# Kernel tuning notes

Hardware: AMD Instinct MI355X
Metric: run time of the kernel (lower is better)

## Reference

```python
import jax, jax.numpy as jnp
import numpy as np
import math

B, S, HID, H = 4, 1024, 1024, 16
DH = HID // H

def setup_inputs() -> dict:
    key = jax.random.key(0)
    ks = jax.random.split(key, 16)
    inp = {
        'q': jax.random.normal(ks[0], (B, S, HID), jnp.float32),
        'k': jax.random.normal(ks[1], (B, S, HID), jnp.float32),
        'v': jax.random.normal(ks[2], (B, S, HID), jnp.float32),
        'k_b': jax.random.normal(ks[3], (B, S, HID), jnp.float32),
        'mask': jax.random.randint(ks[4], (B, S), 0, 2, jnp.int32),
    }
    sc = 1.0 / math.sqrt(HID)
    names = ['Wq', 'Wk', 'Wv', 'Wkb', 'Wo']
    for i, n in enumerate(names):
        inp[n] = jax.random.normal(ks[5 + i], (HID, HID), jnp.float32) * sc
        inp['b' + n[1:]] = jnp.zeros((HID,), jnp.float32)
    return inp

def _split_heads(x):
    # [B,S,HID] -> [B,H,S,DH]
    return x.reshape(B, S, H, DH).transpose(0, 2, 1, 3)

def reference(q, k, v, k_b, mask, Wq, bq, Wk, bk, Wv, bv, Wkb, bkb, Wo, bo):
    qh = _split_heads(q @ Wq.T + bq)
    kh = _split_heads(k @ Wk.T + bk)
    vh = _split_heads(v @ Wv.T + bv)
    kbh = _split_heads(k_b @ Wkb.T + bkb)
    scale = 1.0 / math.sqrt(3 * DH)
    # Q@K^T + Q@Kb^T == Q@(K+Kb)^T
    corr = jnp.einsum('bhsd,bhtd->bhst', qh, kh + kbh) * scale
    # mask[b,j] broadcast over heads and query positions
    corr = jnp.where(mask[:, None, None, :] == 0, jnp.float32(-1e9), corr)
    prob = jax.nn.softmax(corr, axis=-1)  # dropout p=0 (eval)
    hidden = jnp.einsum('bhst,bhtd->bhsd', prob, vh)
    hidden = hidden.transpose(0, 2, 1, 3).reshape(B, S, HID)
    return hidden @ Wo.T + bo
```

## Files before the change

kernel.cpp:

```cpp
#include <hip/hip_runtime.h>
#include <hip/hip_bf16.h>
#include <stdint.h>

#define B_   4
#define S_   1024
#define HID_ 1024
#define H_   16
#define DH_  64

typedef short bf16x8 __attribute__((ext_vector_type(8)));
typedef float f32x4  __attribute__((ext_vector_type(4)));
typedef unsigned int u32;
typedef unsigned short u16;

typedef u32 __attribute__((address_space(1))) as1_u32;
typedef u32 __attribute__((address_space(3))) as3_u32;

__device__ __forceinline__ f32x4 mfma16(bf16x8 a, bf16x8 b, f32x4 c) {
  return __builtin_amdgcn_mfma_f32_16x16x32_bf16(a, b, c, 0, 0, 0);
}

__device__ __forceinline__ void gload16(const void* g, void* l) {
  __builtin_amdgcn_global_load_lds((const as1_u32*)g, (as3_u32*)l, 16, 0, 0);
}

__device__ __forceinline__ u16 f2bf(float f) {
  __hip_bfloat16 h = __float2bfloat16(f);
  union { __hip_bfloat16 h; u16 u; } cv; cv.h = h; return cv.u;
}

__device__ __forceinline__ u32 cvtpk(float lo, float hi) {
  u32 r;
  asm("v_cvt_pk_bf16_f32 %0, %1, %2" : "=v"(r) : "v"(lo), "v"(hi));
  return r;
}

__global__ __launch_bounds__(256) void cvt_all(
    const float* a0, const float* a1, const float* a2, const float* a3,
    const float* w0, const float* w1, const float* w2, const float* w3, const float* w4,
    u16* da0, u16* da1, u16* da2, u16* da3,
    u16* dw0, u16* dw1, u16* dw2, u16* dw3, u16* dw4) {
  int bb = blockIdx.x;
  const float* s; u16* d; size_t i;
  if (bb < 8192) {
    int t = bb * 256 + threadIdx.x;
    int sel = t >> 19;
    i = (size_t)(t & 524287) * 8;
    if (sel == 0)      { s = a0; d = da0; }
    else if (sel == 1) { s = a1; d = da1; }
    else if (sel == 2) { s = a2; d = da2; }
    else               { s = a3; d = da3; }
  } else {
    int t = (bb - 8192) * 256 + threadIdx.x;
    int sel = t >> 17;
    i = (size_t)(t & 131071) * 8;
    if (sel == 0)      { s = w0; d = dw0; }
    else if (sel == 1) { s = w1; d = dw1; }
    else if (sel == 2) { s = w2; d = dw2; }
    else if (sel == 3) { s = w3; d = dw3; }
    else               { s = w4; d = dw4; }
  }
  float4 v0 = *(const float4*)(s + i);
  float4 v1 = *(const float4*)(s + i + 4);
  uint4 r;
  r.x = cvtpk(v0.x, v0.y);
  r.y = cvtpk(v0.z, v0.w);
  r.z = cvtpk(v1.x, v1.y);
  r.w = cvtpk(v1.z, v1.w);
  *(uint4*)(d + i) = r;
}

__global__ __launch_bounds__(256) void gemm_proj(
    const u16* __restrict__ qbf, const u16* __restrict__ Wqbf,
    const u16* __restrict__ kbf, const u16* __restrict__ Wkbf,
    const u16* __restrict__ kbbf, const u16* __restrict__ Wkbbf,
    const u16* __restrict__ vbf, const u16* __restrict__ Wvbf,
    const float* __restrict__ bq, const float* __restrict__ bk,
    const float* __restrict__ bkb, const float* __restrict__ bv,
    u16* __restrict__ Qp, u16* __restrict__ KKp, u16* __restrict__ Vtp) {
  __shared__ __align__(16) char smem[32768];
  const int tid = threadIdx.x;
  const int lane = tid & 63, w = tid >> 6;
  const int g = lane >> 4, ql = lane & 15;
  const int wm = w >> 1, wn = w & 1;
  const int xr = ql & 7;
  const int logical = (blockIdx.x & 7) * 128 + (blockIdx.x >> 3);

  if (logical < 512) {
    const int m0 = (logical >> 4) * 128;
    const int n0 = (logical & 15) * 64;
    f32x4 acc[4][2];
    #pragma unroll
    for (int mi = 0; mi < 4; ++mi)
      #pragma unroll
      for (int ni = 0; ni < 2; ++ni) acc[mi][ni] = f32x4{0.f, 0.f, 0.f, 0.f};

    for (int kt = 0; kt < 32; ++kt) {
      const u16* As = (kt < 16) ? kbf : kbbf;
      const u16* Ws = (kt < 16) ? Wkbf : Wkbbf;
      const int kk = (kt & 15) * 64;
      #pragma unroll
      for (int is = 0; is < 4; ++is) {
        int o = is * 4096 + tid * 16;
        int row = o >> 7, ch = (o >> 4) & 7;
        gload16(As + (size_t)(m0 + row) * HID_ + kk + ((ch ^ (row & 7)) * 8),
                smem + is * 4096 + w * 1024);
      }
      #pragma unroll
      for (int is = 0; is < 2; ++is) {
        int o = is * 4096 + tid * 16;
        int row = o >> 7, ch = (o >> 4) & 7;
        gload16(Ws + (size_t)(n0 + row) * HID_ + kk + ((ch ^ (row & 7)) * 8),
                smem + 16384 + is * 4096 + w * 1024);
      }
      __syncthreads();
      bf16x8 af[4][2], bfv[2][2];
      #pragma unroll
      for (int mi = 0; mi < 4; ++mi)
        #pragma unroll
        for (int c = 0; c < 2; ++c) {
          int row = wm * 64 + mi * 16 + ql;
          af[mi][c] = *(const bf16x8*)(smem + row * 128 + (((c * 4 + g) ^ xr) * 16));
        }
      #pragma unroll
      for (int ni = 0; ni < 2; ++ni)
        #pragma unroll
        for (int c = 0; c < 2; ++c) {
          int row = wn * 32 + ni * 16 + ql;
          bfv[ni][c] = *(const bf16x8*)(smem + 16384 + row * 128 + (((c * 4 + g) ^ xr) * 16));
        }
      #pragma unroll
      for (int c = 0; c < 2; ++c)
        #pragma unroll
        for (int mi = 0; mi < 4; ++mi)
          #pragma unroll
          for (int ni = 0; ni < 2; ++ni)
            acc[mi][ni] = mfma16(af[mi][c], bfv[ni][c], acc[mi][ni]);
      __syncthreads();
    }
    #pragma unroll
    for (int ni = 0; ni < 2; ++ni) {
      int n = n0 + wn * 32 + ni * 16 + ql;
      float bs = bk[n] + bkb[n];
      #pragma unroll
      for (int mi = 0; mi < 4; ++mi)
        #pragma unroll
        for (int i = 0; i < 4; ++i) {
          int m = m0 + wm * 64 + mi * 16 + g * 4 + i;
          KKp[(size_t)m * HID_ + n] = f2bf(acc[mi][ni][i] + bs);
        }
    }
    return;
  }

  const int unit = (logical - 512) >> 8;
  const int bidu = logical & 255;
  const int m0 = (bidu >> 3) * 128;
  const int n0 = (bidu & 7) * 128;
  const u16* A0 = unit ? vbf : qbf;
  const u16* W0 = unit ? Wvbf : Wqbf;
  const float* b0 = unit ? bv : bq;
  const float osc = unit ? 1.f : 0.07216878364870322f * 1.44269504088896340f;

  f32x4 acc[4][4];
  #pragma unroll
  for (int mi = 0; mi < 4; ++mi)
    #pragma unroll
    for (int ni = 0; ni < 4; ++ni) acc[mi][ni] = f32x4{0.f, 0.f, 0.f, 0.f};

  for (int kt = 0; kt < 16; ++kt) {
    const int kk = kt * 64;
    #pragma unroll
    for (int is = 0; is < 4; ++is) {
      int o = is * 4096 + tid * 16;
      int row = o >> 7, ch = (o >> 4) & 7;
      gload16(A0 + (size_t)(m0 + row) * HID_ + kk + ((ch ^ (row & 7)) * 8),
              smem + is * 4096 + w * 1024);
      gload16(W0 + (size_t)(n0 + row) * HID_ + kk + ((ch ^ (row & 7)) * 8),
              smem + 16384 + is * 4096 + w * 1024);
    }
    __syncthreads();
    bf16x8 af[4][2], bfv[4][2];
    #pragma unroll
    for (int mi = 0; mi < 4; ++mi)
      #pragma unroll
      for (int c = 0; c < 2; ++c) {
        int row = wm * 64 + mi * 16 + ql;
        af[mi][c] = *(const bf16x8*)(smem + row * 128 + (((c * 4 + g) ^ xr) * 16));
      }
    #pragma unroll
    for (int ni = 0; ni < 4; ++ni)
      #pragma unroll
      for (int c = 0; c < 2; ++c) {
        int row = wn * 64 + ni * 16 + ql;
        bfv[ni][c] = *(const bf16x8*)(smem + 16384 + row * 128 + (((c * 4 + g) ^ xr) * 16));
      }
    #pragma unroll
    for (int c = 0; c < 2; ++c)
      #pragma unroll
      for (int mi = 0; mi < 4; ++mi)
        #pragma unroll
        for (int ni = 0; ni < 4; ++ni)
          acc[mi][ni] = mfma16(af[mi][c], bfv[ni][c], acc[mi][ni]);
    __syncthreads();
  }

  if (unit == 0) {
    #pragma unroll
    for (int ni = 0; ni < 4; ++ni) {
      int n = n0 + wn * 64 + ni * 16 + ql;
      float bs = b0[n];
      #pragma unroll
      for (int mi = 0; mi < 4; ++mi)
        #pragma unroll
        for (int i = 0; i < 4; ++i) {
          int m = m0 + wm * 64 + mi * 16 + g * 4 + i;
          Qp[(size_t)m * HID_ + n] = f2bf((acc[mi][ni][i] + bs) * osc);
        }
    }
  } else {
    char* tp = smem + w * 8192;
    #pragma unroll
    for (int ni = 0; ni < 4; ++ni) {
      int n = n0 + wn * 64 + ni * 16 + ql;
      float bs = b0[n];
      #pragma unroll
      for (int mi = 0; mi < 4; ++mi)
        #pragma unroll
        for (int i = 0; i < 4; ++i) {
          int nl = ni * 16 + ql;
          int ml = mi * 16 + g * 4 + i;
          *(u16*)(tp + nl * 128 + (((ml >> 3) ^ (nl & 7)) * 16) + (ml & 7) * 2) =
              f2bf(acc[mi][ni][i] + bs);
        }
    }
    __syncthreads();
    int nl = lane;
    int n = n0 + wn * 64 + nl;
    int h = n >> 6, dh = n & 63;
    int mb = m0 + wm * 64;
    int b = mb >> 10, s0 = mb & 1023;
    int bh = b * H_ + h;
    u16* orow = Vtp + (((size_t)(bh * DH_ + dh)) << 10) + s0;
    #pragma unroll
    for (int j = 0; j < 8; ++j) {
      uint4 val = *(const uint4*)(tp + nl * 128 + ((j ^ (nl & 7)) * 16));
      *(uint4*)(orow + j * 8) = val;
    }
  }
}

__global__ __launch_bounds__(256) void gemm_o(const u16* __restrict__ A0, const u16* __restrict__ W0,
                                              const float* __restrict__ bias0, float* __restrict__ outp) {
  __shared__ __align__(16) char smem[24576];
  const int tid = threadIdx.x;
  const int lane = tid & 63, w = tid >> 6;
  const int g = lane >> 4, ql = lane & 15;
  const int wm = w >> 1, wn = w & 1;
  const int logical = (blockIdx.x & 7) * 64 + (blockIdx.x >> 3);
  const int m0 = (logical >> 4) * 128;
  const int n0 = (logical & 15) * 64;
  const int xr = ql & 7;

  f32x4 acc[4][2];
  #pragma unroll
  for (int mi = 0; mi < 4; ++mi)
    #pragma unroll
    for (int ni = 0; ni < 2; ++ni) acc[mi][ni] = f32x4{0.f, 0.f, 0.f, 0.f};

  for (int kt = 0; kt < 16; ++kt) {
    const int kk = kt * 64;
    #pragma unroll
    for (int is = 0; is < 4; ++is) {
      int o = is * 4096 + tid * 16;
      int row = o >> 7, ch = (o >> 4) & 7;
      gload16(A0 + (size_t)(m0 + row) * HID_ + kk + ((ch ^ (row & 7)) * 8),
              smem + is * 4096 + w * 1024);
    }
    #pragma unroll
    for (int is = 0; is < 2; ++is) {
      int o = is * 4096 + tid * 16;
      int row = o >> 7, ch = (o >> 4) & 7;
      gload16(W0 + (size_t)(n0 + row) * HID_ + kk + ((ch ^ (row & 7)) * 8),
              smem + 16384 + is * 4096 + w * 1024);
    }
    __syncthreads();
    bf16x8 af[4][2], bfv[2][2];
    #pragma unroll
    for (int mi = 0; mi < 4; ++mi)
      #pragma unroll
      for (int c = 0; c < 2; ++c) {
        int row = wm * 64 + mi * 16 + ql;
        af[mi][c] = *(const bf16x8*)(smem + row * 128 + (((c * 4 + g) ^ xr) * 16));
      }
    #pragma unroll
    for (int ni = 0; ni < 2; ++ni)
      #pragma unroll
      for (int c = 0; c < 2; ++c) {
        int row = wn * 32 + ni * 16 + ql;
        bfv[ni][c] = *(const bf16x8*)(smem + 16384 + row * 128 + (((c * 4 + g) ^ xr) * 16));
      }
    #pragma unroll
    for (int c = 0; c < 2; ++c)
      #pragma unroll
      for (int mi = 0; mi < 4; ++mi)
        #pragma unroll
        for (int ni = 0; ni < 2; ++ni)
          acc[mi][ni] = mfma16(af[mi][c], bfv[ni][c], acc[mi][ni]);
    __syncthreads();
  }

  #pragma unroll
  for (int ni = 0; ni < 2; ++ni) {
    int n = n0 + wn * 32 + ni * 16 + ql;
    float bs = bias0[n];
    #pragma unroll
    for (int mi = 0; mi < 4; ++mi)
      #pragma unroll
      for (int i = 0; i < 4; ++i) {
        int m = m0 + wm * 64 + mi * 16 + g * 4 + i;
        outp[(size_t)m * HID_ + n] = acc[mi][ni][i] + bs;
      }
  }
}

__global__ __launch_bounds__(256, 4) void attn(const u16* __restrict__ Qp, const u16* __restrict__ KKp,
                                               const u16* __restrict__ Vt, const int* __restrict__ mask,
                                               u16* __restrict__ hidden) {
  __shared__ __align__(16) char smem[40960];
  const int tid = threadIdx.x;
  const int lane = tid & 63, w = tid >> 6;
  const int g = lane >> 4, ql = lane & 15;
  const int bid = blockIdx.x;
  const int bh = (bid & 7) * 8 + ((bid >> 3) & 7);
  const int qt = bid >> 6;
  const int b = bh >> 4, h = bh & 15;
  const int q0 = qt * 64;
  const int xr = ql & 7;

  #pragma unroll
  for (int is = 0; is < 2; ++is) {
    int o = is * 4096 + tid * 16;
    int row = o >> 7, ch = (o >> 4) & 7;
    gload16(KKp + (size_t)(b * S_ + row) * HID_ + h * DH_ + ((ch ^ (row & 7)) * 8),
            smem + is * 4096 + w * 1024);
    gload16(Vt + (size_t)(bh * DH_ + row) * S_ + ((ch ^ (row & 7)) * 8),
            smem + 8192 + is * 4096 + w * 1024);
  }

  const u16* qrow = Qp + (size_t)(b * S_ + q0 + w * 16 + ql) * HID_ + h * DH_;
  bf16x8 qb0 = *(const bf16x8*)(qrow + g * 8);
  bf16x8 qb1 = *(const bf16x8*)(qrow + 32 + g * 8);
  const int* maskp = mask + b * S_;

  f32x4 oacc[4];
  #pragma unroll
  for (int d = 0; d < 4; ++d) oacc[d] = f32x4{0.f, 0.f, 0.f, 0.f};
  float m_run = -1e30f, l_run = 0.f;
  char* pbase = smem + 32768 + w * 2048 + ql * 128;

  int pb = 0;
  for (int it = 0; it < 16; ++it) {
    const int k0 = it * 64;
    int4 mv[4];
    #pragma unroll
    for (int t = 0; t < 4; ++t) mv[t] = *(const int4*)(maskp + k0 + 16 * t + 4 * g);
    __builtin_amdgcn_sched_barrier(0);
    if (it < 15) {
      const int k0s = k0 + 64;
      const int bo = (pb ^ 1) * 16384;
      #pragma unroll
      for (int is = 0; is < 2; ++is) {
        int o = is * 4096 + tid * 16;
        int row = o >> 7, ch = (o >> 4) & 7;
        gload16(KKp + (size_t)(b * S_ + k0s + row) * HID_ + h * DH_ + ((ch ^ (row & 7)) * 8),
                smem + bo + is * 4096 + w * 1024);
        gload16(Vt + (size_t)(bh * DH_ + row) * S_ + k0s + ((ch ^ (row & 7)) * 8),
                smem + bo + 8192 + is * 4096 + w * 1024);
      }
      asm volatile("s_waitcnt vmcnt(4)" ::: "memory");
    } else {
      asm volatile("s_waitcnt vmcnt(0)" ::: "memory");
    }
    __builtin_amdgcn_s_barrier();

    const char* kb_ = smem + pb * 16384;
    const char* vb_ = smem + pb * 16384 + 8192;

    float sv[4][4];
    #pragma unroll
    for (int t = 0; t < 4; ++t) {
      const char* krow = kb_ + (16 * t + ql) * 128;
      bf16x8 ka0 = *(const bf16x8*)(krow + ((g ^ xr) * 16));
      bf16x8 ka1 = *(const bf16x8*)(krow + (((4 + g) ^ xr) * 16));
      f32x4 st = mfma16(ka0, qb0, f32x4{0.f, 0.f, 0.f, 0.f});
      st = mfma16(ka1, qb1, st);
      sv[t][0] = mv[t].x ? st[0] : -1e9f;
      sv[t][1] = mv[t].y ? st[1] : -1e9f;
      sv[t][2] = mv[t].z ? st[2] : -1e9f;
      sv[t][3] = mv[t].w ? st[3] : -1e9f;
    }
    float mloc = sv[0][0];
    #pragma unroll
    for (int t = 0; t < 4; ++t)
      #pragma unroll
      for (int i = 0; i < 4; ++i) mloc = fmaxf(mloc, sv[t][i]);
    mloc = fmaxf(mloc, __shfl_xor(mloc, 16, 64));
    mloc = fmaxf(mloc, __shfl_xor(mloc, 32, 64));
    if (__any(mloc > m_run + 10.f)) {
      float mnew = fmaxf(m_run, mloc);
      float alpha = __builtin_amdgcn_exp2f(m_run - mnew);
      l_run *= alpha;
      #pragma unroll
      for (int d = 0; d < 4; ++d) oacc[d] *= alpha;
      m_run = mnew;
    }
    float rsum = 0.f;
    float pvs[4][4];
    #pragma unroll
    for (int t = 0; t < 4; ++t)
      #pragma unroll
      for (int i = 0; i < 4; ++i) {
        float p = __builtin_amdgcn_exp2f(sv[t][i] - m_run);
        pvs[t][i] = p; rsum += p;
      }
    rsum += __shfl_xor(rsum, 16, 64);
    rsum += __shfl_xor(rsum, 32, 64);
    l_run += rsum;

    #pragma unroll
    for (int t = 0; t < 4; ++t) {
      uint2 pw;
      pw.x = cvtpk(pvs[t][0], pvs[t][1]);
      pw.y = cvtpk(pvs[t][2], pvs[t][3]);
      *(uint2*)(pbase + (((4 * t + g) ^ (2 * xr)) * 8)) = pw;
    }
    #pragma unroll
    for (int c = 0; c < 2; ++c) {
      bf16x8 pf = *(const bf16x8*)(pbase + (((c * 4 + g) ^ xr) * 16));
      #pragma unroll
      for (int d = 0; d < 4; ++d) {
        bf16x8 va = *(const bf16x8*)(vb_ + (16 * d + ql) * 128 + (((c * 4 + g) ^ xr) * 16));
        oacc[d] = mfma16(va, pf, oacc[d]);
      }
    }
    __builtin_amdgcn_s_barrier();
    pb ^= 1;
  }

  float inv = 1.0f / l_run;
  char* ep = smem + w * 2304;
  #pragma unroll
  for (int d = 0; d < 4; ++d)
    #pragma unroll
    for (int i = 0; i < 4; ++i)
      *(u16*)(ep + ql * 144 + (16 * d + 4 * g + i) * 2) = f2bf(oacc[d][i] * inv);
  __syncthreads();
  int r = lane >> 2, cc = lane & 3;
  const char* erow = smem + w * 2304 + r * 144 + cc * 32;
  uint4 v0 = *(const uint4*)erow;
  uint4 v1 = *(const uint4*)(erow + 16);
  u16* orow = hidden + (size_t)(b * S_ + q0 + w * 16 + r) * HID_ + h * DH_ + cc * 16;
  *(uint4*)orow = v0;
  *(uint4*)(orow + 8) = v1;
}

extern "C" void kernel_launch(void* const* d_in, const int* in_sizes, int n_in,
                              void* d_out, int out_size, void* d_ws, size_t ws_size,
                              hipStream_t stream) {
  (void)in_sizes; (void)n_in; (void)out_size; (void)ws_size;
  const float* q    = (const float*)d_in[0];
  const float* k    = (const float*)d_in[1];
  const float* v    = (const float*)d_in[2];
  const float* kb   = (const float*)d_in[3];
  const int*   mask = (const int*)  d_in[4];
  const float* Wq   = (const float*)d_in[5];
  const float* bq   = (const float*)d_in[6];
  const float* Wk   = (const float*)d_in[7];
  const float* bk   = (const float*)d_in[8];
  const float* Wv   = (const float*)d_in[9];
  const float* bv   = (const float*)d_in[10];
  const float* Wkb  = (const float*)d_in[11];
  const float* bkb  = (const float*)d_in[12];
  const float* Wo   = (const float*)d_in[13];
  const float* bo   = (const float*)d_in[14];

  char* ws = (char*)d_ws;
  const size_t MB = 1024 * 1024;
  u16* qbf   = (u16*)(ws + 0 * MB);
  u16* kbf   = (u16*)(ws + 8 * MB);
  u16* vbf   = (u16*)(ws + 16 * MB);
  u16* kbbf  = (u16*)(ws + 24 * MB);
  u16* Wqbf  = (u16*)(ws + 32 * MB);
  u16* Wkbf  = (u16*)(ws + 34 * MB);
  u16* Wvbf  = (u16*)(ws + 36 * MB);
  u16* Wkbbf = (u16*)(ws + 38 * MB);
  u16* Wobf  = (u16*)(ws + 40 * MB);
  u16* Qp    = (u16*)(ws + 42 * MB);
  u16* KKp   = (u16*)(ws + 50 * MB);
  u16* Vtp   = (u16*)(ws + 58 * MB);
  u16* hid   = (u16*)(ws + 66 * MB);

  cvt_all<<<10752, 256, 0, stream>>>(q, k, v, kb, Wq, Wk, Wv, Wkb, Wo,
                                     qbf, kbf, vbf, kbbf, Wqbf, Wkbf, Wvbf, Wkbbf, Wobf);
  gemm_proj<<<1024, 256, 0, stream>>>(qbf, Wqbf, kbf, Wkbf, kbbf, Wkbbf, vbf, Wvbf,
                                      bq, bk, bkb, bv, Qp, KKp, Vtp);
  attn<<<1024, 256, 0, stream>>>(Qp, KKp, Vtp, mask, hid);
  gemm_o<<<512, 256, 0, stream>>>(hid, Wobf, bo, (float*)d_out);
}
```

Before: 127.2 us.

## Fuse fp32-to-bf16 conversion into GEMM loaders with register-staged double buffering

Removes the separate cvt_all kernel. The projection and output GEMMs now read fp32 inputs and weights straight from global memory into registers, convert them to bf16, and write them into swizzled double-buffered LDS, prefetching the next K tile while the current one runs on MFMA. This avoids writing and re-reading bf16 copies of all activations and weights and drops one kernel launch. In exchange, each GEMM reads twice the bytes per tile, uses more registers and doubles its LDS footprint, which may reduce occupancy. It also adds s_setprio hints and manual waitcnt/barrier synchronisation.

```diff
diff --git a/kernel.cpp b/kernel.cpp
--- a/kernel.cpp
+++ b/kernel.cpp
@@ -35,50 +35,48 @@
   return r;
 }
 
-__global__ __launch_bounds__(256) void cvt_all(
-    const float* a0, const float* a1, const float* a2, const float* a3,
-    const float* w0, const float* w1, const float* w2, const float* w3, const float* w4,
-    u16* da0, u16* da1, u16* da2, u16* da3,
-    u16* dw0, u16* dw1, u16* dw2, u16* dw3, u16* dw4) {
-  int bb = blockIdx.x;
-  const float* s; u16* d; size_t i;
-  if (bb < 8192) {
-    int t = bb * 256 + threadIdx.x;
-    int sel = t >> 19;
-    i = (size_t)(t & 524287) * 8;
-    if (sel == 0)      { s = a0; d = da0; }
-    else if (sel == 1) { s = a1; d = da1; }
-    else if (sel == 2) { s = a2; d = da2; }
-    else               { s = a3; d = da3; }
-  } else {
-    int t = (bb - 8192) * 256 + threadIdx.x;
-    int sel = t >> 17;
-    i = (size_t)(t & 131071) * 8;
-    if (sel == 0)      { s = w0; d = dw0; }
-    else if (sel == 1) { s = w1; d = dw1; }
-    else if (sel == 2) { s = w2; d = dw2; }
-    else if (sel == 3) { s = w3; d = dw3; }
-    else               { s = w4; d = dw4; }
-  }
-  float4 v0 = *(const float4*)(s + i);
-  float4 v1 = *(const float4*)(s + i + 4);
-  uint4 r;
-  r.x = cvtpk(v0.x, v0.y);
-  r.y = cvtpk(v0.z, v0.w);
-  r.z = cvtpk(v1.x, v1.y);
-  r.w = cvtpk(v1.z, v1.w);
-  *(uint4*)(d + i) = r;
+__device__ __forceinline__ void lds_publish() {
+  asm volatile("s_waitcnt lgkmcnt(0)" ::: "memory");
+  __builtin_amdgcn_sched_barrier(0);
+  __builtin_amdgcn_s_barrier();
+}
+
+template<int NP>
+__device__ __forceinline__ void load_rows(const float* __restrict__ src, int tid, float4 (&r)[NP][2]) {
+  #pragma unroll
+  for (int j = 0; j < NP; ++j) {
+    int p = j * 256 + tid;
+    int row = p >> 3, pc = p & 7;
+    const float* a = src + (size_t)row * HID_ + pc * 8;
+    r[j][0] = *(const float4*)a;
+    r[j][1] = *(const float4*)(a + 4);
+  }
+}
+
+template<int NP>
+__device__ __forceinline__ void cvt_store(char* base, int tid, const float4 (&r)[NP][2]) {
+  #pragma unroll
+  for (int j = 0; j < NP; ++j) {
+    int p = j * 256 + tid;
+    int row = p >> 3, pc = p & 7;
+    uint4 val;
+    val.x = cvtpk(r[j][0].x, r[j][0].y);
+    val.y = cvtpk(r[j][0].z, r[j][0].w);
+    val.z = cvtpk(r[j][1].x, r[j][1].y);
+    val.w = cvtpk(r[j][1].z, r[j][1].w);
+    *(uint4*)(base + row * 128 + ((pc ^ (row & 7)) * 16)) = val;
+  }
 }
 
 __global__ __launch_bounds__(256) void gemm_proj(
-    const u16* __restrict__ qbf, const u16* __restrict__ Wqbf,
-    const u16* __restrict__ kbf, const u16* __restrict__ Wkbf,
-    const u16* __restrict__ kbbf, const u16* __restrict__ Wkbbf,
-    const u16* __restrict__ vbf, const u16* __restrict__ Wvbf,
+    const float* __restrict__ qf, const float* __restrict__ Wqf,
+    const float* __restrict__ kf, const float* __restrict__ Wkf,
+    const float* __restrict__ kbf_, const float* __restrict__ Wkbf_,
+    const float* __restrict__ vf, const float* __restrict__ Wvf,
     const float* __restrict__ bq, const float* __restrict__ bk,
     const float* __restrict__ bkb, const float* __restrict__ bv,
     u16* __restrict__ Qp, u16* __restrict__ KKp, u16* __restrict__ Vtp) {
-  __shared__ __align__(16) char smem[32768];
+  __shared__ __align__(16) char smem[65536];
   const int tid = threadIdx.x;
   const int lane = tid & 63, w = tid >> 6;
   const int g = lane >> 4, ql = lane & 15;
@@ -95,40 +93,43 @@
       #pragma unroll
       for (int ni = 0; ni < 2; ++ni) acc[mi][ni] = f32x4{0.f, 0.f, 0.f, 0.f};
 
+    float4 ra[4][2], rw[2][2];
+    load_rows<4>(kf + (size_t)m0 * HID_, tid, ra);
+    load_rows<2>(Wkf + (size_t)n0 * HID_, tid, rw);
+
+    #pragma unroll 1
     for (int kt = 0; kt < 32; ++kt) {
-      const u16* As = (kt < 16) ? kbf : kbbf;
-      const u16* Ws = (kt < 16) ? Wkbf : Wkbbf;
-      const int kk = (kt & 15) * 64;
-      #pragma unroll
-      for (int is = 0; is < 4; ++is) {
-        int o = is * 4096 + tid * 16;
-        int row = o >> 7, ch = (o >> 4) & 7;
-        gload16(As + (size_t)(m0 + row) * HID_ + kk + ((ch ^ (row & 7)) * 8),
-                smem + is * 4096 + w * 1024);
-      }
-      #pragma unroll
-      for (int is = 0; is < 2; ++is) {
-        int o = is * 4096 + tid * 16;
-        int row = o >> 7, ch = (o >> 4) & 7;
-        gload16(Ws + (size_t)(n0 + row) * HID_ + kk + ((ch ^ (row & 7)) * 8),
-                smem + 16384 + is * 4096 + w * 1024);
-      }
-      __syncthreads();
+      const int boA = (kt & 1) ? 24576 : 0;
+      const int boW = (kt & 1) ? 40960 : 16384;
+      cvt_store<4>(smem + boA, tid, ra);
+      cvt_store<2>(smem + boW, tid, rw);
+      if (kt < 31) {
+        int kn = kt + 1;
+        const float* As = (kn < 16) ? kf : kbf_;
+        const float* Ws = (kn < 16) ? Wkf : Wkbf_;
+        int kk = (kn & 15) * 64;
+        load_rows<4>(As + (size_t)m0 * HID_ + kk, tid, ra);
+        load_rows<2>(Ws + (size_t)n0 * HID_ + kk, tid, rw);
+      }
+      lds_publish();
+      const char* ab = smem + boA;
+      const char* wb = smem + boW;
       bf16x8 af[4][2], bfv[2][2];
       #pragma unroll
       for (int mi = 0; mi < 4; ++mi)
         #pragma unroll
         for (int c = 0; c < 2; ++c) {
           int row = wm * 64 + mi * 16 + ql;
-          af[mi][c] = *(const bf16x8*)(smem + row * 128 + (((c * 4 + g) ^ xr) * 16));
+          af[mi][c] = *(const bf16x8*)(ab + row * 128 + (((c * 4 + g) ^ xr) * 16));
         }
       #pragma unroll
       for (int ni = 0; ni < 2; ++ni)
         #pragma unroll
         for (int c = 0; c < 2; ++c) {
           int row = wn * 32 + ni * 16 + ql;
-          bfv[ni][c] = *(const bf16x8*)(smem + 16384 + row * 128 + (((c * 4 + g) ^ xr) * 16));
+          bfv[ni][c] = *(const bf16x8*)(wb + row * 128 + (((c * 4 + g) ^ xr) * 16));
         }
+      __builtin_amdgcn_s_setprio(1);
       #pragma unroll
       for (int c = 0; c < 2; ++c)
         #pragma unroll
@@ -136,7 +137,8 @@
           #pragma unroll
           for (int ni = 0; ni < 2; ++ni)
             acc[mi][ni] = mfma16(af[mi][c], bfv[ni][c], acc[mi][ni]);
-      __syncthreads();
+      __builtin_amdgcn_s_setprio(0);
+      __builtin_amdgcn_s_barrier();
     }
     #pragma unroll
     for (int ni = 0; ni < 2; ++ni) {
@@ -157,8 +159,8 @@
   const int bidu = logical & 255;
   const int m0 = (bidu >> 3) * 128;
   const int n0 = (bidu & 7) * 128;
-  const u16* A0 = unit ? vbf : qbf;
-  const u16* W0 = unit ? Wvbf : Wqbf;
+  const float* A0 = unit ? vf : qf;
+  const float* W0 = unit ? Wvf : Wqf;
   const float* b0 = unit ? bv : bq;
   const float osc = unit ? 1.f : 0.07216878364870322f * 1.44269504088896340f;
 
@@ -168,33 +170,40 @@
     #pragma unroll
     for (int ni = 0; ni < 4; ++ni) acc[mi][ni] = f32x4{0.f, 0.f, 0.f, 0.f};
 
+  float4 ra[4][2], rw[4][2];
+  load_rows<4>(A0 + (size_t)m0 * HID_, tid, ra);
+  load_rows<4>(W0 + (size_t)n0 * HID_, tid, rw);
+
+  #pragma unroll 1
   for (int kt = 0; kt < 16; ++kt) {
-    const int kk = kt * 64;
-    #pragma unroll
-    for (int is = 0; is < 4; ++is) {
-      int o = is * 4096 + tid * 16;
-      int row = o >> 7, ch = (o >> 4) & 7;
-      gload16(A0 + (size_t)(m0 + row) * HID_ + kk + ((ch ^ (row & 7)) * 8),
-              smem + is * 4096 + w * 1024);
-      gload16(W0 + (size_t)(n0 + row) * HID_ + kk + ((ch ^ (row & 7)) * 8),
-              smem + 16384 + is * 4096 + w * 1024);
-    }
-    __syncthreads();
+    const int boA = (kt & 1) ? 32768 : 0;
+    const int boW = (kt & 1) ? 49152 : 16384;
+    cvt_store<4>(smem + boA, tid, ra);
+    cvt_store<4>(smem + boW, tid, rw);
+    if (kt < 15) {
+      int kk = (kt + 1) * 64;
+      load_rows<4>(A0 + (size_t)m0 * HID_ + kk, tid, ra);
+      load_rows<4>(W0 + (size_t)n0 * HID_ + kk, tid, rw);
+    }
+    lds_publish();
+    const char* ab = smem + boA;
+    const char* wb = smem + boW;
     bf16x8 af[4][2], bfv[4][2];
     #pragma unroll
     for (int mi = 0; mi < 4; ++mi)
       #pragma unroll
       for (int c = 0; c < 2; ++c) {
         int row = wm * 64 + mi * 16 + ql;
-        af[mi][c] = *(const bf16x8*)(smem + row * 128 + (((c * 4 + g) ^ xr) * 16));
+        af[mi][c] = *(const bf16x8*)(ab + row * 128 + (((c * 4 + g) ^ xr) * 16));
       }
     #pragma unroll
     for (int ni = 0; ni < 4; ++ni)
       #pragma unroll
       for (int c = 0; c < 2; ++c) {
         int row = wn * 64 + ni * 16 + ql;
-        bfv[ni][c] = *(const bf16x8*)(smem + 16384 + row * 128 + (((c * 4 + g) ^ xr) * 16));
-      }
+        bfv[ni][c] = *(const bf16x8*)(wb + row * 128 + (((c * 4 + g) ^ xr) * 16));
+      }
+    __builtin_amdgcn_s_setprio(1);
     #pragma unroll
     for (int c = 0; c < 2; ++c)
       #pragma unroll
@@ -202,7 +211,8 @@
         #pragma unroll
         for (int ni = 0; ni < 4; ++ni)
           acc[mi][ni] = mfma16(af[mi][c], bfv[ni][c], acc[mi][ni]);
-    __syncthreads();
+    __builtin_amdgcn_s_setprio(0);
+    __builtin_amdgcn_s_barrier();
   }
 
   if (unit == 0) {
@@ -250,9 +260,9 @@
   }
 }
 
-__global__ __launch_bounds__(256) void gemm_o(const u16* __restrict__ A0, const u16* __restrict__ W0,
+__global__ __launch_bounds__(256) void gemm_o(const u16* __restrict__ A0, const float* __restrict__ Wof,
                                               const float* __restrict__ bias0, float* __restrict__ outp) {
-  __shared__ __align__(16) char smem[24576];
+  __shared__ __align__(16) char smem[49152];
   const int tid = threadIdx.x;
   const int lane = tid & 63, w = tid >> 6;
   const int g = lane >> 4, ql = lane & 15;
@@ -268,38 +278,53 @@
     #pragma unroll
     for (int ni = 0; ni < 2; ++ni) acc[mi][ni] = f32x4{0.f, 0.f, 0.f, 0.f};
 
+  #pragma unroll
+  for (int is = 0; is < 4; ++is) {
+    int o = is * 4096 + tid * 16;
+    int row = o >> 7, ch = (o >> 4) & 7;
+    gload16(A0 + (size_t)(m0 + row) * HID_ + ((ch ^ (row & 7)) * 8),
+            smem + is * 4096 + w * 1024);
+  }
+  float4 rw[2][2];
+  load_rows<2>(Wof + (size_t)n0 * HID_, tid, rw);
+
+  #pragma unroll 1
   for (int kt = 0; kt < 16; ++kt) {
-    const int kk = kt * 64;
-    #pragma unroll
-    for (int is = 0; is < 4; ++is) {
-      int o = is * 4096 + tid * 16;
-      int row = o >> 7, ch = (o >> 4) & 7;
-      gload16(A0 + (size_t)(m0 + row) * HID_ + kk + ((ch ^ (row & 7)) * 8),
-              smem + is * 4096 + w * 1024);
-    }
-    #pragma unroll
-    for (int is = 0; is < 2; ++is) {
-      int o = is * 4096 + tid * 16;
-      int row = o >> 7, ch = (o >> 4) & 7;
-      gload16(W0 + (size_t)(n0 + row) * HID_ + kk + ((ch ^ (row & 7)) * 8),
-              smem + 16384 + is * 4096 + w * 1024);
-    }
-    __syncthreads();
+    const int boA = (kt & 1) ? 16384 : 0;
+    const int boW = (kt & 1) ? 40960 : 32768;
+    cvt_store<2>(smem + boW, tid, rw);
+    if (kt < 15) load_rows<2>(Wof + (size_t)n0 * HID_ + (kt + 1) * 64, tid, rw);
+    if (kt < 15) asm volatile("s_waitcnt vmcnt(8)" ::: "memory");
+    else         asm volatile("s_waitcnt vmcnt(0)" ::: "memory");
+    lds_publish();
+    if (kt < 15) {
+      int kk = (kt + 1) * 64;
+      #pragma unroll
+      for (int is = 0; is < 4; ++is) {
+        int o = is * 4096 + tid * 16;
+        int row = o >> 7, ch = (o >> 4) & 7;
+        gload16(A0 + (size_t)(m0 + row) * HID_ + kk + ((ch ^ (row & 7)) * 8),
+                smem + ((kt + 1) & 1 ? 16384 : 0) + is * 4096 + w * 1024);
+      }
+    }
+    const char* ab = smem + boA;
+    const char* wb = smem + boW;
     bf16x8 af[4][2], bfv[2][2];
     #pragma unroll
     for (int mi = 0; mi < 4; ++mi)
       #pragma unroll
       for (int c = 0; c < 2; ++c) {
         int row = wm * 64 + mi * 16 + ql;
-        af[mi][c] = *(const bf16x8*)(smem + row * 128 + (((c * 4 + g) ^ xr) * 16));
+        af[mi][c] = *(const bf16x8*)(ab + row * 128 + (((c * 4 + g) ^ xr) * 16));
       }
     #pragma unroll
     for (int ni = 0; ni < 2; ++ni)
       #pragma unroll
       for (int c = 0; c < 2; ++c) {
         int row = wn * 32 + ni * 16 + ql;
-        bfv[ni][c] = *(const bf16x8*)(smem + 16384 + row * 128 + (((c * 4 + g) ^ xr) * 16));
-      }
+        bfv[ni][c] = *(const bf16x8*)(wb + row * 128 + (((c * 4 + g) ^ xr) * 16));
+      }
+    __builtin_amdgcn_s_setprio(1);
     #pragma unroll
     for (int c = 0; c < 2; ++c)
       #pragma unroll
@@ -307,7 +332,8 @@
         #pragma unroll
         for (int ni = 0; ni < 2; ++ni)
           acc[mi][ni] = mfma16(af[mi][c], bfv[ni][c], acc[mi][ni]);
-    __syncthreads();
+    __builtin_amdgcn_s_setprio(0);
+    __builtin_amdgcn_s_barrier();
   }
 
   #pragma unroll
@@ -487,24 +513,13 @@
 
   char* ws = (char*)d_ws;
   const size_t MB = 1024 * 1024;
-  u16* qbf   = (u16*)(ws + 0 * MB);
-  u16* kbf   = (u16*)(ws + 8 * MB);
-  u16* vbf   = (u16*)(ws + 16 * MB);
-  u16* kbbf  = (u16*)(ws + 24 * MB);
-  u16* Wqbf  = (u16*)(ws + 32 * MB);
-  u16* Wkbf  = (u16*)(ws + 34 * MB);
-  u16* Wvbf  = (u16*)(ws + 36 * MB);
-  u16* Wkbbf = (u16*)(ws + 38 * MB);
-  u16* Wobf  = (u16*)(ws + 40 * MB);
-  u16* Qp    = (u16*)(ws + 42 * MB);
-  u16* KKp   = (u16*)(ws + 50 * MB);
-  u16* Vtp   = (u16*)(ws + 58 * MB);
-  u16* hid   = (u16*)(ws + 66 * MB);
-
-  cvt_all<<<10752, 256, 0, stream>>>(q, k, v, kb, Wq, Wk, Wv, Wkb, Wo,
-                                     qbf, kbf, vbf, kbbf, Wqbf, Wkbf, Wvbf, Wkbbf, Wobf);
-  gemm_proj<<<1024, 256, 0, stream>>>(qbf, Wqbf, kbf, Wkbf, kbbf, Wkbbf, vbf, Wvbf,
+  u16* Qp  = (u16*)(ws + 0 * MB);
+  u16* KKp = (u16*)(ws + 8 * MB);
+  u16* Vtp = (u16*)(ws + 16 * MB);
+  u16* hid = (u16*)(ws + 24 * MB);
+
+  gemm_proj<<<1024, 256, 0, stream>>>(q, Wq, k, Wk, kb, Wkb, v, Wv,
                                       bq, bk, bkb, bv, Qp, KKp, Vtp);
   attn<<<1024, 256, 0, stream>>>(Qp, KKp, Vtp, mask, hid);
-  gemm_o<<<512, 256, 0, stream>>>(hid, Wobf, bo, (float*)d_out);
-}
+  gemm_o<<<512, 256, 0, stream>>>(hid, Wo, bo, (float*)d_out);
+}
```

After: 131.3 us. 1.03x slower.

## Double-buffer LDS tiles in projection and output GEMMs with async prefetch

Applied to the files above, without the earlier changes.

Both the projection GEMM and the output GEMM now double-buffer their LDS tiles. The next k-tile's global_load_lds is issued before the current tile is computed, and partial vmcnt waits let the loads overlap the MFMA work. The change also raises wave priority around the MFMA blocks and remaps the projection block index so each XCD gets a contiguous range of tiles. The cost is doubled LDS per block, which can lower occupancy, plus hand-written waitcnt counts that must exactly match the number of loads issued.

```diff
diff --git a/kernel.cpp b/kernel.cpp
--- a/kernel.cpp
+++ b/kernel.cpp
@@ -33,6 +33,18 @@
   u32 r;
   asm("v_cvt_pk_bf16_f32 %0, %1, %2" : "=v"(r) : "v"(lo), "v"(hi));
   return r;
+}
+
+template<int NC>
+__device__ __forceinline__ void stage_tile(const u16* __restrict__ src, char* smem, int bo,
+                                           int tid, int w) {
+  #pragma unroll
+  for (int is = 0; is < NC; ++is) {
+    int o = is * 4096 + tid * 16;
+    int row = o >> 7, ch = (o >> 4) & 7;
+    gload16(src + (size_t)row * HID_ + ((ch ^ (row & 7)) * 8),
+            smem + bo + is * 4096 + w * 1024);
+  }
 }
 
 __global__ __launch_bounds__(256) void cvt_all(
@@ -78,57 +90,61 @@
     const float* __restrict__ bq, const float* __restrict__ bk,
     const float* __restrict__ bkb, const float* __restrict__ bv,
     u16* __restrict__ Qp, u16* __restrict__ KKp, u16* __restrict__ Vtp) {
-  __shared__ __align__(16) char smem[32768];
+  __shared__ __align__(16) char smem[65536];
   const int tid = threadIdx.x;
   const int lane = tid & 63, w = tid >> 6;
   const int g = lane >> 4, ql = lane & 15;
   const int wm = w >> 1, wn = w & 1;
   const int xr = ql & 7;
-  const int logical = (blockIdx.x & 7) * 128 + (blockIdx.x >> 3);
-
-  if (logical < 512) {
-    const int m0 = (logical >> 4) * 128;
-    const int n0 = (logical & 15) * 64;
+  const int xcd = blockIdx.x & 7, idx = blockIdx.x >> 3;
+
+  if (idx < 64) {
+    const int kkid = xcd * 64 + idx;
+    const int m0 = (kkid >> 4) * 128;
+    const int n0 = (kkid & 15) * 64;
     f32x4 acc[4][2];
     #pragma unroll
     for (int mi = 0; mi < 4; ++mi)
       #pragma unroll
       for (int ni = 0; ni < 2; ++ni) acc[mi][ni] = f32x4{0.f, 0.f, 0.f, 0.f};
 
+    stage_tile<4>(kbf + (size_t)m0 * HID_, smem, 0, tid, w);
+    stage_tile<2>(Wkbf + (size_t)n0 * HID_, smem, 16384, tid, w);
+
+    #pragma unroll 1
     for (int kt = 0; kt < 32; ++kt) {
-      const u16* As = (kt < 16) ? kbf : kbbf;
-      const u16* Ws = (kt < 16) ? Wkbf : Wkbbf;
-      const int kk = (kt & 15) * 64;
-      #pragma unroll
-      for (int is = 0; is < 4; ++is) {
-        int o = is * 4096 + tid * 16;
-        int row = o >> 7, ch = (o >> 4) & 7;
-        gload16(As + (size_t)(m0 + row) * HID_ + kk + ((ch ^ (row & 7)) * 8),
-                smem + is * 4096 + w * 1024);
-      }
-      #pragma unroll
-      for (int is = 0; is < 2; ++is) {
-        int o = is * 4096 + tid * 16;
-        int row = o >> 7, ch = (o >> 4) & 7;
-        gload16(Ws + (size_t)(n0 + row) * HID_ + kk + ((ch ^ (row & 7)) * 8),
-                smem + 16384 + is * 4096 + w * 1024);
-      }
-      __syncthreads();
+      const int boA = (kt & 1) ? 32768 : 0;
+      const int boW = (kt & 1) ? 49152 : 16384;
+      if (kt < 31) {
+        int kn = kt + 1;
+        const u16* As = (kn < 16) ? kbf : kbbf;
+        const u16* Ws = (kn < 16) ? Wkbf : Wkbbf;
+        int kk = (kn & 15) * 64;
+        stage_tile<4>(As + (size_t)m0 * HID_ + kk, smem, boA ^ 32768, tid, w);
+        stage_tile<2>(Ws + (size_t)n0 * HID_ + kk, smem, boW ^ (16384 ^ 49152), tid, w);
+        asm volatile("s_waitcnt vmcnt(6)" ::: "memory");
+      } else {
+        asm volatile("s_waitcnt vmcnt(0)" ::: "memory");
+      }
+      __builtin_amdgcn_s_barrier();
+      const char* ab = smem + boA;
+      const char* wb = smem + boW;
       bf16x8 af[4][2], bfv[2][2];
       #pragma unroll
       for (int mi = 0; mi < 4; ++mi)
         #pragma unroll
         for (int c = 0; c < 2; ++c) {
           int row = wm * 64 + mi * 16 + ql;
-          af[mi][c] = *(const bf16x8*)(smem + row * 128 + (((c * 4 + g) ^ xr) * 16));
+          af[mi][c] = *(const bf16x8*)(ab + row * 128 + (((c * 4 + g) ^ xr) * 16));
         }
       #pragma unroll
       for (int ni = 0; ni < 2; ++ni)
         #pragma unroll
         for (int c = 0; c < 2; ++c) {
           int row = wn * 32 + ni * 16 + ql;
-          bfv[ni][c] = *(const bf16x8*)(smem + 16384 + row * 128 + (((c * 4 + g) ^ xr) * 16));
+          bfv[ni][c] = *(const bf16x8*)(wb + row * 128 + (((c * 4 + g) ^ xr) * 16));
         }
+      __builtin_amdgcn_s_setprio(1);
       #pragma unroll
       for (int c = 0; c < 2; ++c)
         #pragma unroll
@@ -136,7 +152,8 @@
           #pragma unroll
           for (int ni = 0; ni < 2; ++ni)
             acc[mi][ni] = mfma16(af[mi][c], bfv[ni][c], acc[mi][ni]);
-      __syncthreads();
+      __builtin_amdgcn_s_setprio(0);
+      __builtin_amdgcn_s_barrier();
     }
     #pragma unroll
     for (int ni = 0; ni < 2; ++ni) {
@@ -153,10 +170,10 @@
     return;
   }
 
-  const int unit = (logical - 512) >> 8;
-  const int bidu = logical & 255;
-  const int m0 = (bidu >> 3) * 128;
-  const int n0 = (bidu & 7) * 128;
+  const int unit = (idx < 96) ? 0 : 1;
+  const int uid = xcd * 32 + (idx & 31);
+  const int m0 = (uid >> 3) * 128;
+  const int n0 = (uid & 7) * 128;
   const u16* A0 = unit ? vbf : qbf;
   const u16* W0 = unit ? Wvbf : Wqbf;
   const float* b0 = unit ? bv : bq;
@@ -168,33 +185,40 @@
     #pragma unroll
     for (int ni = 0; ni < 4; ++ni) acc[mi][ni] = f32x4{0.f, 0.f, 0.f, 0.f};
 
+  stage_tile<4>(A0 + (size_t)m0 * HID_, smem, 0, tid, w);
+  stage_tile<4>(W0 + (size_t)n0 * HID_, smem, 16384, tid, w);
+
+  #pragma unroll 1
   for (int kt = 0; kt < 16; ++kt) {
-    const int kk = kt * 64;
-    #pragma unroll
-    for (int is = 0; is < 4; ++is) {
-      int o = is * 4096 + tid * 16;
-      int row = o >> 7, ch = (o >> 4) & 7;
-      gload16(A0 + (size_t)(m0 + row) * HID_ + kk + ((ch ^ (row & 7)) * 8),
-              smem + is * 4096 + w * 1024);
-      gload16(W0 + (size_t)(n0 + row) * HID_ + kk + ((ch ^ (row & 7)) * 8),
-              smem + 16384 + is * 4096 + w * 1024);
-    }
-    __syncthreads();
+    const int boA = (kt & 1) ? 32768 : 0;
+    const int boW = (kt & 1) ? 49152 : 16384;
+    if (kt < 15) {
+      int kk = (kt + 1) * 64;
+      stage_tile<4>(A0 + (size_t)m0 * HID_ + kk, smem, boA ^ 32768, tid, w);
+      stage_tile<4>(W0 + (size_t)n0 * HID_ + kk, smem, boW ^ (16384 ^ 49152), tid, w);
+      asm volatile("s_waitcnt vmcnt(8)" ::: "memory");
+    } else {
+      asm volatile("s_waitcnt vmcnt(0)" ::: "memory");
+    }
+    __builtin_amdgcn_s_barrier();
+    const char* ab = smem + boA;
+    const char* wb = smem + boW;
     bf16x8 af[4][2], bfv[4][2];
     #pragma unroll
     for (int mi = 0; mi < 4; ++mi)
       #pragma unroll
       for (int c = 0; c < 2; ++c) {
         int row = wm * 64 + mi * 16 + ql;
-        af[mi][c] = *(const bf16x8*)(smem + row * 128 + (((c * 4 + g) ^ xr) * 16));
+        af[mi][c] = *(const bf16x8*)(ab + row * 128 + (((c * 4 + g) ^ xr) * 16));
       }
     #pragma unroll
     for (int ni = 0; ni < 4; ++ni)
       #pragma unroll
       for (int c = 0; c < 2; ++c) {
         int row = wn * 64 + ni * 16 + ql;
-        bfv[ni][c] = *(const bf16x8*)(smem + 16384 + row * 128 + (((c * 4 + g) ^ xr) * 16));
-      }
+        bfv[ni][c] = *(const bf16x8*)(wb + row * 128 + (((c * 4 + g) ^ xr) * 16));
+      }
+    __builtin_amdgcn_s_setprio(1);
     #pragma unroll
     for (int c = 0; c < 2; ++c)
       #pragma unroll
@@ -202,7 +226,8 @@
         #pragma unroll
         for (int ni = 0; ni < 4; ++ni)
           acc[mi][ni] = mfma16(af[mi][c], bfv[ni][c], acc[mi][ni]);
-    __syncthreads();
+    __builtin_amdgcn_s_setprio(0);
+    __builtin_amdgcn_s_barrier();
   }
 
   if (unit == 0) {
@@ -252,7 +277,7 @@
 
 __global__ __launch_bounds__(256) void gemm_o(const u16* __restrict__ A0, const u16* __restrict__ W0,
                                               const float* __restrict__ bias0, float* __restrict__ outp) {
-  __shared__ __align__(16) char smem[24576];
+  __shared__ __align__(16) char smem[49152];
   const int tid = threadIdx.x;
   const int lane = tid & 63, w = tid >> 6;
   const int g = lane >> 4, ql = lane & 15;
@@ -268,38 +293,40 @@
     #pragma unroll
     for (int ni = 0; ni < 2; ++ni) acc[mi][ni] = f32x4{0.f, 0.f, 0.f, 0.f};
 
+  stage_tile<4>(A0 + (size_t)m0 * HID_, smem, 0, tid, w);
+  stage_tile<2>(W0 + (size_t)n0 * HID_, smem, 32768, tid, w);
+
+  #pragma unroll 1
   for (int kt = 0; kt < 16; ++kt) {
-    const int kk = kt * 64;
-    #pragma unroll
-    for (int is = 0; is < 4; ++is) {
-      int o = is * 4096 + tid * 16;
-      int row = o >> 7, ch = (o >> 4) & 7;
-      gload16(A0 + (size_t)(m0 + row) * HID_ + kk + ((ch ^ (row & 7)) * 8),
-              smem + is * 4096 + w * 1024);
-    }
-    #pragma unroll
-    for (int is = 0; is < 2; ++is) {
-      int o = is * 4096 + tid * 16;
-      int row = o >> 7, ch = (o >> 4) & 7;
-      gload16(W0 + (size_t)(n0 + row) * HID_ + kk + ((ch ^ (row & 7)) * 8),
-              smem + 16384 + is * 4096 + w * 1024);
-    }
-    __syncthreads();
+    const int boA = (kt & 1) ? 16384 : 0;
+    const int boW = (kt & 1) ? 40960 : 32768;
+    if (kt < 15) {
+      int kk = (kt + 1) * 64;
+      stage_tile<4>(A0 + (size_t)m0 * HID_ + kk, smem, boA ^ 16384, tid, w);
+      stage_tile<2>(W0 + (size_t)n0 * HID_ + kk, smem, boW ^ (32768 ^ 40960), tid, w);
+      asm volatile("s_waitcnt vmcnt(6)" ::: "memory");
+    } else {
+      asm volatile("s_waitcnt vmcnt(0)" ::: "memory");
+    }
+    __builtin_amdgcn_s_barrier();
+    const char* ab = smem + boA;
+    const char* wb = smem + boW;
     bf16x8 af[4][2], bfv[2][2];
     #pragma unroll
     for (int mi = 0; mi < 4; ++mi)
       #pragma unroll
       for (int c = 0; c < 2; ++c) {
         int row = wm * 64 + mi * 16 + ql;
-        af[mi][c] = *(const bf16x8*)(smem + row * 128 + (((c * 4 + g) ^ xr) * 16));
+        af[mi][c] = *(const bf16x8*)(ab + row * 128 + (((c * 4 + g) ^ xr) * 16));
       }
     #pragma unroll
     for (int ni = 0; ni < 2; ++ni)
       #pragma unroll
       for (int c = 0; c < 2; ++c) {
         int row = wn * 32 + ni * 16 + ql;
-        bfv[ni][c] = *(const bf16x8*)(smem + 16384 + row * 128 + (((c * 4 + g) ^ xr) * 16));
-      }
+        bfv[ni][c] = *(const bf16x8*)(wb + row * 128 + (((c * 4 + g) ^ xr) * 16));
+      }
+    __builtin_amdgcn_s_setprio(1);
     #pragma unroll
     for (int c = 0; c < 2; ++c)
       #pragma unroll
@@ -307,7 +334,8 @@
         #pragma unroll
         for (int ni = 0; ni < 2; ++ni)
           acc[mi][ni] = mfma16(af[mi][c], bfv[ni][c], acc[mi][ni]);
-    __syncthreads();
+    __builtin_amdgcn_s_setprio(0);
+    __builtin_amdgcn_s_barrier();
   }
 
   #pragma unroll
```

Result: faster. 123.1 us (-3.2%).
